# Performance work log

Hardware: AMD Instinct MI355X
Metric: run time of the kernel (lower is better)

## Reference

```python
import jax, jax.numpy as jnp
import numpy as np

S_INIT, S_FINAL = 512, 1024
LAYER_DIM, NEXT_DIM, DIM = 512, 512, 1024
BATCH = 32768


def setup_inputs() -> dict:
    rng = np.random.default_rng(0)
    # eigenvector block (trainable 'base') and its 0/1 mask
    base = np.zeros((DIM, DIM), dtype=np.float32)
    base[S_INIT:S_FINAL, S_INIT - LAYER_DIM:S_INIT] = rng.uniform(
        -0.2, 0.2, (NEXT_DIM, LAYER_DIM)).astype(np.float32)
    base_mask = np.zeros((DIM, DIM), dtype=np.float32)
    base_mask[S_INIT:S_FINAL, S_INIT - LAYER_DIM:S_INIT] = 1.0
    eye = np.eye(DIM, dtype=np.float32)
    # eigenvalue diagonal block; NOTE: trainable_diag_mask holds the *random values*
    # (not 0/1), exactly as in the original TF code.
    masks = np.zeros((DIM, DIM), dtype=np.float32)
    masks[S_INIT:S_FINAL, S_INIT:S_FINAL] = np.diag(
        rng.uniform(-1.8, 1.8, NEXT_DIM).astype(np.float32))
    untrainable_diag = eye - masks
    trainable_diag = masks.copy()
    trainable_diag_mask = masks.copy()
    # column masks selecting pass-through rows vs. activated block rows
    mask1 = np.ones((DIM, 1), dtype=np.float32)
    mask1[S_INIT:S_FINAL] = 0.0
    mask2 = np.zeros((DIM, 1), dtype=np.float32)
    mask2[S_INIT:S_FINAL] = 1.0

    key = jax.random.key(0)
    data = jax.random.normal(key, (BATCH, DIM), dtype=jnp.float32)
    return {
        "data": data,
        "base": jnp.asarray(base),
        "base_mask": jnp.asarray(base_mask),
        "eye": jnp.asarray(eye),
        "trainable_diag": jnp.asarray(trainable_diag),
        "trainable_diag_mask": jnp.asarray(trainable_diag_mask),
        "untrainable_diag": jnp.asarray(untrainable_diag),
        "mask1": jnp.asarray(mask1),
        "mask2": jnp.asarray(mask2),
    }


def reference(data, base, base_mask, eye, trainable_diag, trainable_diag_mask,
              untrainable_diag, mask1, mask2):
    # layer = masked base + I ; diag = masked trainable diag + (I - fixed diag)
    layer = base * base_mask + eye                                  # [D, D]
    diag = trainable_diag * trainable_diag_mask + untrainable_diag  # [D, D]
    x = jnp.matmul(2.0 * eye - layer, data.T)                       # [D, B]
    x = jnp.matmul(diag, x)                                         # [D, B]
    x = jnp.matmul(layer, x)                                        # [D, B]
    temp = jax.nn.relu(x)  # relu is elementwise; transpose pair cancels
    x = x * mask1 + temp * mask2                                    # [D, B]
    return x.T                                                      # [B, D]
```

## Files before the change

kernel.cpp:

```cpp
#include <hip/hip_runtime.h>


typedef float f32x4 __attribute__((ext_vector_type(4)));
typedef int   i32x4 __attribute__((ext_vector_type(4)));

#define DIMW   1024
#define HALFD  512
#define BM     64
#define LDAP   520
#define NITER  16
#define NCOPY  256

__device__ __forceinline__ unsigned short f2bf(float x) {
    union { float f; unsigned int i; } c;
    c.f = x;
    unsigned int r = c.i + 0x7FFFu + ((c.i >> 16) & 1u);
    return (unsigned short)(r >> 16);
}
__device__ __forceinline__ unsigned int pack2(float a, float b) {
    return (unsigned int)f2bf(a) | ((unsigned int)f2bf(b) << 16);
}

__device__ __forceinline__ void mfma_16x16x32_bf16(f32x4& d, const i32x4& a, const i32x4& b) {
    asm volatile("v_mfma_f32_16x16x32_bf16 %0, %1, %2, %0"
                 : "+v"(d)
                 : "v"(a), "v"(b));
}
__device__ __forceinline__ void acc_fence(f32x4& d) {
    asm volatile("s_nop 7\n\ts_nop 7" : "+v"(d));
}

__global__ __launch_bounds__(512, 4) void spectral_kernel(
    const float* __restrict__ data,
    const float* __restrict__ wsrc,
    const float* __restrict__ td,
    const float* __restrict__ tdm,
    const float* __restrict__ ud,
    float* __restrict__ out)
{
    const int tid = (int)threadIdx.x;

    if ((int)blockIdx.x < NCOPY) {
        const int rowBase = (int)blockIdx.x * 128;
        const float4* src = (const float4*)data;
        float4*       dst = (float4*)out;
        #pragma unroll
        for (int h = 0; h < 4; ++h) {
            float4 v[8];
            #pragma unroll
            for (int p = 0; p < 8; ++p) {
                int c  = (h * 8 + p) * 512 + tid;
                int r  = c >> 7;
                int cc = c & 127;
                v[p] = src[(size_t)(rowBase + r) * (DIMW / 4) + cc];
            }
            #pragma unroll
            for (int p = 0; p < 8; ++p) {
                int c  = (h * 8 + p) * 512 + tid;
                int r  = c >> 7;
                int cc = c & 127;
                dst[(size_t)(rowBase + r) * (DIMW / 4) + cc] = v[p];
            }
        }
        return;
    }

    __shared__ unsigned short As[BM * LDAP];
    __shared__ float dsh[HALFD];

    const int lane   = tid & 63;
    const int wn     = tid >> 6;
    const int lane16 = lane & 15;
    const int quad   = lane >> 4;
    const int rowBase = ((int)blockIdx.x - NCOPY) * BM;

    {
        int j = HALFD + tid;
        size_t fi = (size_t)j * DIMW + j;
        dsh[tid] = td[fi] * tdm[fi] + ud[fi];
    }

    #pragma unroll
    for (int h = 0; h < 2; ++h) {
        float4 v[8];
        #pragma unroll
        for (int p = 0; p < 8; ++p) {
            int c  = (h * 8 + p) * 512 + tid;
            int r  = c >> 7;
            int cc = c & 127;
            v[p] = *(const float4*)(data + (size_t)(rowBase + r) * DIMW + cc * 4);
        }
        #pragma unroll
        for (int p = 0; p < 8; ++p) {
            int c  = (h * 8 + p) * 512 + tid;
            int r  = c >> 7;
            int cc = c & 127;
            uint2 uu;
            uu.x = pack2(v[p].x, v[p].y);
            uu.y = pack2(v[p].z, v[p].w);
            *(uint2*)(As + r * LDAP + cc * 4) = uu;
        }
    }

    i32x4 b0[4], b1[4];

    auto LDW = [&](int it, i32x4 (&b)[4]) {
        #pragma unroll
        for (int ni = 0; ni < 4; ++ni) {
            int col = wn * 64 + ni * 16 + lane16;
            const float* p = wsrc + (size_t)(HALFD + col) * DIMW + it * 32 + quad * 8;
            float4 f0 = *(const float4*)p;
            float4 f1 = *(const float4*)(p + 4);
            i32x4 t;
            t[0] = (int)pack2(f0.x, f0.y);  t[1] = (int)pack2(f0.z, f0.w);
            t[2] = (int)pack2(f1.x, f1.y);  t[3] = (int)pack2(f1.z, f1.w);
            b[ni] = t;
        }
    };

    LDW(0, b0);
    LDW(1, b1);
    __syncthreads();

    f32x4 acc[4][4];
    #pragma unroll
    for (int mi = 0; mi < 4; ++mi)
        #pragma unroll
        for (int ni = 0; ni < 4; ++ni)
            acc[mi][ni] = (f32x4){0.f, 0.f, 0.f, 0.f};

    auto STEP = [&](int it, i32x4 (&b)[4]) {
        i32x4 a[4];
        #pragma unroll
        for (int mi = 0; mi < 4; ++mi)
            a[mi] = *(const i32x4*)(As + (mi * 16 + lane16) * LDAP + it * 32 + quad * 8);
        #pragma unroll
        for (int mi = 0; mi < 4; ++mi)
            #pragma unroll
            for (int ni = 0; ni < 4; ++ni)
                mfma_16x16x32_bf16(acc[mi][ni], b[ni], a[mi]);
    };

    #pragma unroll
    for (int it = 0; it < NITER; it += 2) {
        STEP(it, b0);
        if (it + 2 < NITER) LDW(it + 2, b0);
        STEP(it + 1, b1);
        if (it + 3 < NITER) LDW(it + 3, b1);
    }

    #pragma unroll
    for (int mi = 0; mi < 4; ++mi)
        #pragma unroll
        for (int ni = 0; ni < 4; ++ni)
            acc_fence(acc[mi][ni]);

    #pragma unroll
    for (int mi = 0; mi < 4; ++mi) {
        const int row = rowBase + mi * 16 + lane16;
        const float* drow = data + (size_t)row * DIMW + HALFD;
        float*       orow = out  + (size_t)row * DIMW + HALFD;
        #pragma unroll
        for (int ni = 0; ni < 4; ++ni) {
            const int colb = wn * 64 + ni * 16 + quad * 4;
            float4 u1 = *(const float4*)(drow + colb);
            float4 d4 = *(const float4*)(dsh + colb);
            float4 o;
            o.x = fmaxf(d4.x * u1.x + (1.0f - d4.x) * acc[mi][ni][0], 0.0f);
            o.y = fmaxf(d4.y * u1.y + (1.0f - d4.y) * acc[mi][ni][1], 0.0f);
            o.z = fmaxf(d4.z * u1.z + (1.0f - d4.z) * acc[mi][ni][2], 0.0f);
            o.w = fmaxf(d4.w * u1.w + (1.0f - d4.w) * acc[mi][ni][3], 0.0f);
            *(float4*)(orow + colb) = o;
        }
    }
}

extern "C" void kernel_launch(void* const* d_in, const int* in_sizes, int n_in,
                              void* d_out, int out_size, void* d_ws, size_t ws_size,
                              hipStream_t stream) {
    const float* data = (const float*)d_in[0];
    const float* base = (const float*)d_in[1];
    const float* td   = (const float*)d_in[4];
    const float* tdm  = (const float*)d_in[5];
    const float* ud   = (const float*)d_in[6];
    float* out = (float*)d_out;

    dim3 block(512, 1, 1);
    dim3 grid(NCOPY + 32768 / BM, 1, 1);
    spectral_kernel<<<grid, block, 0, stream>>>(data, base, td, tdm, ud, out);
}
```

Baseline: 346.8 us.

## Fold pass-through half copy into GEMM blocks, interleaved with MFMA loop

Result: slower. 405.4 us (+16.9%).

```diff
diff --git a/kernel.cpp b/kernel.cpp
--- a/kernel.cpp
+++ b/kernel.cpp
@@ -9,7 +9,6 @@
 #define BM     64
 #define LDAP   520
 #define NITER  16
-#define NCOPY  256
 
 __device__ __forceinline__ unsigned short f2bf(float x) {
     union { float f; unsigned int i; } c;
@@ -38,41 +37,15 @@
     const float* __restrict__ ud,
     float* __restrict__ out)
 {
-    const int tid = (int)threadIdx.x;
-
-    if ((int)blockIdx.x < NCOPY) {
-        const int rowBase = (int)blockIdx.x * 128;
-        const float4* src = (const float4*)data;
-        float4*       dst = (float4*)out;
-        #pragma unroll
-        for (int h = 0; h < 4; ++h) {
-            float4 v[8];
-            #pragma unroll
-            for (int p = 0; p < 8; ++p) {
-                int c  = (h * 8 + p) * 512 + tid;
-                int r  = c >> 7;
-                int cc = c & 127;
-                v[p] = src[(size_t)(rowBase + r) * (DIMW / 4) + cc];
-            }
-            #pragma unroll
-            for (int p = 0; p < 8; ++p) {
-                int c  = (h * 8 + p) * 512 + tid;
-                int r  = c >> 7;
-                int cc = c & 127;
-                dst[(size_t)(rowBase + r) * (DIMW / 4) + cc] = v[p];
-            }
-        }
-        return;
-    }
-
     __shared__ unsigned short As[BM * LDAP];
     __shared__ float dsh[HALFD];
 
+    const int tid    = (int)threadIdx.x;
     const int lane   = tid & 63;
     const int wn     = tid >> 6;
     const int lane16 = lane & 15;
     const int quad   = lane >> 4;
-    const int rowBase = ((int)blockIdx.x - NCOPY) * BM;
+    const int rowBase = (int)blockIdx.x * BM;
 
     {
         int j = HALFD + tid;
@@ -141,13 +114,34 @@
                 mfma_16x16x32_bf16(acc[mi][ni], b[ni], a[mi]);
     };
 
+    float4 cp[NITER];
+    auto CPL = [&](int it) {
+        int c  = it * 512 + tid;
+        int r  = c >> 7;
+        int cc = c & 127;
+        cp[it] = *(const float4*)(data + (size_t)(rowBase + r) * DIMW + cc * 4);
+    };
+    auto CPS = [&](int it) {
+        int c  = it * 512 + tid;
+        int r  = c >> 7;
+        int cc = c & 127;
+        *(float4*)(out + (size_t)(rowBase + r) * DIMW + cc * 4) = cp[it];
+    };
+
     #pragma unroll
-    for (int it = 0; it < NITER; it += 2) {
+    for (int ib = 0; ib < 8; ++ib) {
+        const int it = ib * 2;
+        CPL(it);
         STEP(it, b0);
         if (it + 2 < NITER) LDW(it + 2, b0);
+        if (it >= 2) CPS(it - 2);
+        CPL(it + 1);
         STEP(it + 1, b1);
         if (it + 3 < NITER) LDW(it + 3, b1);
+        if (it >= 2) CPS(it - 1);
     }
+    CPS(14);
+    CPS(15);
 
     #pragma unroll
     for (int mi = 0; mi < 4; ++mi)
@@ -186,6 +180,6 @@
     float* out = (float*)d_out;
 
     dim3 block(512, 1, 1);
-    dim3 grid(NCOPY + 32768 / BM, 1, 1);
+    dim3 grid(32768 / BM, 1, 1);
     spectral_kernel<<<grid, block, 0, stream>>>(data, base, td, tdm, ud, out);
 }
```
